# Performance work log

Hardware: AMD Instinct MI355X
Metric: run time of the kernel (lower is better)

Reference implementation:

```python
import jax, jax.numpy as jnp
import numpy as np

D_MODEL, N_HEADS, D_K = 768, 12, 64
LN_EPS = 1e-5


def setup_inputs() -> dict:
    key = jax.random.key(0)
    ks = jax.random.split(key, 8)
    b, c, n, s = 8, 32, 4, 64
    scale = 1.0 / np.sqrt(D_MODEL)
    inp = {
        "e": jax.random.normal(ks[0], (b, c, n, s, D_MODEL), dtype=jnp.float32),
        "h": jax.random.normal(ks[1], (b, c, s, D_MODEL), dtype=jnp.float32),
        # weights stored [in, out] (torch Linear transposed)
        "Wq": jax.random.normal(ks[2], (D_MODEL, N_HEADS * D_K), dtype=jnp.float32) * scale,
        "bq": jnp.zeros((N_HEADS * D_K,), dtype=jnp.float32),
        "Wk": jax.random.normal(ks[3], (D_MODEL, N_HEADS * D_K), dtype=jnp.float32) * scale,
        "bk": jnp.zeros((N_HEADS * D_K,), dtype=jnp.float32),
        "Wv": jax.random.normal(ks[4], (D_MODEL, N_HEADS * D_K), dtype=jnp.float32) * scale,
        "bv": jnp.zeros((N_HEADS * D_K,), dtype=jnp.float32),
        "Wo": jax.random.normal(ks[5], (N_HEADS * D_K, D_MODEL), dtype=jnp.float32) * scale,
        "bo": jnp.zeros((D_MODEL,), dtype=jnp.float32),
        "ln_g": jnp.ones((D_MODEL,), dtype=jnp.float32),
        "ln_b": jnp.zeros((D_MODEL,), dtype=jnp.float32),
    }
    return inp


def _layer_norm(x, g, b):
    mu = jnp.mean(x, axis=-1, keepdims=True)
    var = jnp.mean(jnp.square(x - mu), axis=-1, keepdims=True)
    return (x - mu) * jax.lax.rsqrt(var + LN_EPS) * g + b


def reference(e, h, Wq, bq, Wk, bk, Wv, bv, Wo, bo, ln_g, ln_b):
    # e: [b, c, n, i, d]  h: [b, c, j, d]
    e_res = e
    en = _layer_norm(e, ln_g, ln_b)
    b, c, n, i, _ = e.shape
    j = h.shape[2]
    q = (en @ Wq + bq).reshape(b, c, n, i, N_HEADS, D_K)
    k = (h @ Wk + bk).reshape(b, c, j, N_HEADS, D_K)
    v = (h @ Wv + bv).reshape(b, c, j, N_HEADS, D_K)
    attn = jnp.einsum('bcnihd,bcjhd->bcnhij', q, k) * (1.0 / np.sqrt(D_K))
    attn = jax.nn.softmax(attn, axis=-1)
    o = jnp.einsum('bcnhij,bcjhd->bcnihd', attn, v).reshape(b, c, n, i, N_HEADS * D_K)
    return o @ Wo + bo + e_res
```

## Files before the change

### kernel.cpp

```cpp
#include <hip/hip_runtime.h>

typedef __bf16 bf16x8 __attribute__((ext_vector_type(8)));
typedef __bf16 bf16x4 __attribute__((ext_vector_type(4)));
typedef float f32x4 __attribute__((ext_vector_type(4)));

__device__ __forceinline__ f32x4 mfma16(bf16x8 a, bf16x8 b, f32x4 c) {
  return __builtin_amdgcn_mfma_f32_16x16x32_bf16(a, b, c, 0, 0, 0);
}

__device__ __forceinline__ void load_lds16(const void* g, void* l) {
  __builtin_amdgcn_global_load_lds(
      (const __attribute__((address_space(1))) void*)g,
      (__attribute__((address_space(3))) void*)l, 16, 0, 0);
}

template <int NWG>
__device__ __forceinline__ int xcd_swz(int orig) {
  constexpr int NX = 8;
  constexpr int q = NWG / NX;
  constexpr int r = NWG % NX;
  const int xcd = orig % NX;
  const int pos = orig / NX;
  if constexpr (r == 0) {
    return xcd * q + pos;
  } else {
    return (xcd < r ? xcd * (q + 1) : r * (q + 1) + (xcd - r) * q) + pos;
  }
}

__global__ __launch_bounds__(256) void prep_w_kernel(
    const float* __restrict__ Wq, const float* __restrict__ Wk,
    const float* __restrict__ Wv, const float* __restrict__ Wo,
    __bf16* __restrict__ WqT, __bf16* __restrict__ WkvT, __bf16* __restrict__ WoT) {
  __shared__ float tile[32][33];
  const int z = blockIdx.z;
  const float* W = (z == 0) ? Wq : (z == 1) ? Wk : (z == 2) ? Wv : Wo;
  __bf16* out = (z == 0) ? WqT : (z == 3) ? WoT : WkvT;
  const int rowOff = (z == 2) ? 768 : 0;
  const int tx = threadIdx.x, ty = threadIdx.y;
  const int x = blockIdx.x * 32 + tx;
  const int y = blockIdx.y * 32 + ty;
#pragma unroll
  for (int i = 0; i < 32; i += 8) tile[ty + i][tx] = W[(size_t)(y + i) * 768 + x];
  __syncthreads();
  const int nx = blockIdx.y * 32 + tx;
  const int ny = blockIdx.x * 32 + ty;
#pragma unroll
  for (int i = 0; i < 32; i += 8)
    out[(size_t)(rowOff + ny + i) * 768 + nx] = (__bf16)tile[tx][ty + i];
}

__global__ __launch_bounds__(256) void ln_kernel(
    const float* __restrict__ e, const float* __restrict__ gam,
    const float* __restrict__ bet, __bf16* __restrict__ en) {
  const int lane = threadIdx.x & 63;
  const int wid = threadIdx.x >> 6;
  const size_t row = (size_t)blockIdx.x * 4 + wid;
  const float* p = e + row * 768;
  float x[12];
  float sum = 0.f;
#pragma unroll
  for (int s = 0; s < 3; ++s) {
    f32x4 v = *(const f32x4*)(p + (s * 64 + lane) * 4);
#pragma unroll
    for (int q = 0; q < 4; ++q) { x[s * 4 + q] = v[q]; sum += v[q]; }
  }
#pragma unroll
  for (int d = 1; d < 64; d <<= 1) sum += __shfl_xor(sum, d);
  const float m = sum * (1.f / 768.f);
  float vs = 0.f;
#pragma unroll
  for (int q = 0; q < 12; ++q) { float d = x[q] - m; vs += d * d; }
#pragma unroll
  for (int d = 1; d < 64; d <<= 1) vs += __shfl_xor(vs, d);
  const float rr = rsqrtf(vs * (1.f / 768.f) + 1e-5f);
  __bf16* o = en + row * 768;
#pragma unroll
  for (int s = 0; s < 3; ++s) {
    f32x4 g4 = *(const f32x4*)(gam + (s * 64 + lane) * 4);
    f32x4 b4 = *(const f32x4*)(bet + (s * 64 + lane) * 4);
    bf16x4 pk;
#pragma unroll
    for (int q = 0; q < 4; ++q) pk[q] = (__bf16)((x[s * 4 + q] - m) * rr * g4[q] + b4[q]);
    *(bf16x4*)(o + (s * 64 + lane) * 4) = pk;
  }
}

__global__ __launch_bounds__(256) void cast_kernel(
    const float* __restrict__ in, __bf16* __restrict__ out, int n4) {
  int i = blockIdx.x * 256 + threadIdx.x;
  const int stride = gridDim.x * 256;
  for (; i < n4; i += stride) {
    f32x4 v = ((const f32x4*)in)[i];
    bf16x4 o;
#pragma unroll
    for (int q = 0; q < 4; ++q) o[q] = (__bf16)v[q];
    ((bf16x4*)out)[i] = o;
  }
}

enum { MODE_Q = 0, MODE_KV = 1, MODE_O = 2 };

template <int MODE, int NC, int NWG>
__global__ __launch_bounds__(256) void gemm_kernel(
    const __bf16* __restrict__ A,
    const __bf16* __restrict__ WT,
    const float* __restrict__ bias0, const float* __restrict__ bias1,
    const float* __restrict__ eres,
    __bf16* __restrict__ dst0, __bf16* __restrict__ dst1,
    float* __restrict__ outp) {
  __shared__ __bf16 As[2][8192];
  __shared__ __bf16 Bs[2][8192];
  const int wgid = xcd_swz<NWG>(blockIdx.x);
  const int rowBase = (wgid / NC) * 128;
  const int colBase = (wgid % NC) * 128;
  const int t = threadIdx.x;
  const int lane = t & 63, wid = t >> 6;
  const int wm = wid >> 1, wn = wid & 1;
  const int lr = lane & 15, lg = lane >> 4;
  const int srow = lane >> 3;
  const int skcol = ((lane & 7) ^ srow) * 8;
  f32x4 acc[4][4] = {};

  auto stage = [&](int kbb, int buf) {
#pragma unroll
    for (int s = 0; s < 4; ++s) {
      const int chunk = s * 4 + wid;
      const int rowIn = chunk * 8 + srow;
      const __bf16* ga;
      if constexpr (MODE == MODE_O) {
        const int r = rowBase + rowIn;
        ga = A + ((((size_t)(r >> 6)) * 12 + kbb) << 12) + ((r & 63) << 6) + skcol;
      } else {
        ga = A + (size_t)(rowBase + rowIn) * 768 + kbb * 64 + skcol;
      }
      load_lds16(ga, &As[buf][chunk * 512]);
      const __bf16* gb = WT + (size_t)(colBase + rowIn) * 768 + kbb * 64 + skcol;
      load_lds16(gb, &Bs[buf][chunk * 512]);
    }
  };
  auto compute = [&](int buf) {
#pragma unroll
    for (int kc = 0; kc < 2; ++kc) {
      bf16x8 a[4], b[4];
      const int c8 = (kc * 4 + lg) ^ (lr & 7);
#pragma unroll
      for (int it = 0; it < 4; ++it)
        a[it] = *(const bf16x8*)&As[buf][(wm * 64 + it * 16 + lr) * 64 + c8 * 8];
#pragma unroll
      for (int jt = 0; jt < 4; ++jt)
        b[jt] = *(const bf16x8*)&Bs[buf][(wn * 64 + jt * 16 + lr) * 64 + c8 * 8];
#pragma unroll
      for (int it = 0; it < 4; ++it)
#pragma unroll
        for (int jt = 0; jt < 4; ++jt)
          acc[it][jt] = mfma16(a[it], b[jt], acc[it][jt]);
    }
  };

  stage(0, 0);
  stage(1, 1);
#pragma unroll
  for (int kb = 0; kb < 12; ++kb) {
    if (kb < 11) {
      asm volatile("s_waitcnt vmcnt(8)" ::: "memory");
    } else {
      asm volatile("s_waitcnt vmcnt(0)" ::: "memory");
    }
    __builtin_amdgcn_sched_barrier(0);
    __builtin_amdgcn_s_barrier();
    compute(kb & 1);
    __builtin_amdgcn_s_barrier();
    if (kb < 10) stage(kb + 2, kb & 1);
  }

  const int roww = rowBase + wm * 64;
  const int colw = colBase + wn * 64;
#pragma unroll
  for (int it = 0; it < 4; ++it) {
#pragma unroll
    for (int jt = 0; jt < 4; ++jt) {
      const int c = colw + jt * 16 + lr;
#pragma unroll
      for (int rg = 0; rg < 4; ++rg) {
        const int r = roww + it * 16 + lg * 4 + rg;
        const float val = acc[it][jt][rg];
        if constexpr (MODE == MODE_O) {
          outp[(size_t)r * 768 + c] = val + bias0[c] + eres[(size_t)r * 768 + c];
        } else if constexpr (MODE == MODE_Q) {
          dst0[((((size_t)(r >> 6)) * 12 + (c >> 6)) << 12) + ((r & 63) << 6) + (c & 63)] =
              (__bf16)(val + bias0[c]);
        } else {
          if (c < 768) {
            dst0[((((size_t)(r >> 6)) * 12 + (c >> 6)) << 12) + ((r & 63) << 6) + (c & 63)] =
                (__bf16)(val + bias0[c]);
          } else {
            const int c2 = c - 768;
            dst1[((((size_t)(r >> 6)) * 12 + (c2 >> 6)) << 12) + ((c2 & 63) << 6) + (r & 63)] =
                (__bf16)(val + bias1[c2]);
          }
        }
      }
    }
  }
}

__global__ __launch_bounds__(64) void attn_kernel(
    const __bf16* __restrict__ q, const __bf16* __restrict__ k,
    const __bf16* __restrict__ v, __bf16* __restrict__ o) {
  const int gid = xcd_swz<12288>(blockIdx.x);
  const int n = gid & 3;
  const int bh = gid >> 2;
  const int h = bh % 12;
  const int bc = bh / 12;
  const __bf16* qp = q + (((size_t)(bc * 4 + n) * 12 + h) << 12);
  const __bf16* kp = k + (((size_t)bc * 12 + h) << 12);
  const __bf16* vp = v + (((size_t)bc * 12 + h) << 12);
  __bf16* op = o + (((size_t)(bc * 4 + n) * 12 + h) << 12);
  const int lane = threadIdx.x;
  const int lr = lane & 15, lg = lane >> 4;
  __shared__ __bf16 P[64][72];

  bf16x8 qf[4][2], kf[4][2];
#pragma unroll
  for (int it = 0; it < 4; ++it)
#pragma unroll
    for (int kc = 0; kc < 2; ++kc)
      qf[it][kc] = *(const bf16x8*)(qp + (it * 16 + lr) * 64 + kc * 32 + lg * 8);
#pragma unroll
  for (int jt = 0; jt < 4; ++jt)
#pragma unroll
    for (int kc = 0; kc < 2; ++kc)
      kf[jt][kc] = *(const bf16x8*)(kp + (jt * 16 + lr) * 64 + kc * 32 + lg * 8);

  f32x4 s[4][4] = {};
#pragma unroll
  for (int kc = 0; kc < 2; ++kc)
#pragma unroll
    for (int jt = 0; jt < 4; ++jt)
#pragma unroll
      for (int it = 0; it < 4; ++it)
        s[jt][it] = mfma16(kf[jt][kc], qf[it][kc], s[jt][it]);

  float recip[4];
#pragma unroll
  for (int it = 0; it < 4; ++it) {
    float m = -1e30f;
#pragma unroll
    for (int jt = 0; jt < 4; ++jt)
#pragma unroll
      for (int rg = 0; rg < 4; ++rg) m = fmaxf(m, s[jt][it][rg]);
    m = fmaxf(m, __shfl_xor(m, 16));
    m = fmaxf(m, __shfl_xor(m, 32));
    float sum = 0.f;
#pragma unroll
    for (int jt = 0; jt < 4; ++jt) {
      bf16x4 pk;
#pragma unroll
      for (int rg = 0; rg < 4; ++rg) {
        float p = __expf((s[jt][it][rg] - m) * 0.125f);
        sum += p;
        pk[rg] = (__bf16)p;
      }
      *(bf16x4*)&P[it * 16 + lr][jt * 16 + lg * 4] = pk;
    }
    sum += __shfl_xor(sum, 16);
    sum += __shfl_xor(sum, 32);
    recip[it] = 1.f / sum;
  }
  __syncthreads();

  bf16x8 vf[4][2];
#pragma unroll
  for (int dt = 0; dt < 4; ++dt)
#pragma unroll
    for (int kc = 0; kc < 2; ++kc)
      vf[dt][kc] = *(const bf16x8*)(vp + (dt * 16 + lr) * 64 + kc * 32 + lg * 8);
  f32x4 oacc[4][4] = {};
#pragma unroll
  for (int kc = 0; kc < 2; ++kc) {
    bf16x8 pf[4];
#pragma unroll
    for (int it = 0; it < 4; ++it)
      pf[it] = *(const bf16x8*)&P[it * 16 + lr][kc * 32 + lg * 8];
#pragma unroll
    for (int dt = 0; dt < 4; ++dt)
#pragma unroll
      for (int it = 0; it < 4; ++it)
        oacc[dt][it] = mfma16(vf[dt][kc], pf[it], oacc[dt][it]);
  }
#pragma unroll
  for (int it = 0; it < 4; ++it) {
    const float rc = recip[it];
#pragma unroll
    for (int dt = 0; dt < 4; ++dt) {
      bf16x4 pk;
#pragma unroll
      for (int rg = 0; rg < 4; ++rg) pk[rg] = (__bf16)(oacc[dt][it][rg] * rc);
      *(bf16x4*)(op + (size_t)(it * 16 + lr) * 64 + dt * 16 + lg * 4) = pk;
    }
  }
}

extern "C" void kernel_launch(void* const* d_in, const int* in_sizes, int n_in,
                              void* d_out, int out_size, void* d_ws, size_t ws_size,
                              hipStream_t stream) {
  const float* e  = (const float*)d_in[0];
  const float* h  = (const float*)d_in[1];
  const float* Wq = (const float*)d_in[2];
  const float* bq = (const float*)d_in[3];
  const float* Wk = (const float*)d_in[4];
  const float* bk = (const float*)d_in[5];
  const float* Wv = (const float*)d_in[6];
  const float* bv = (const float*)d_in[7];
  const float* Wo = (const float*)d_in[8];
  const float* bo = (const float*)d_in[9];
  const float* g  = (const float*)d_in[10];
  const float* b  = (const float*)d_in[11];
  float* outp = (float*)d_out;
  char* ws = (char*)d_ws;

  __bf16* WqT  = (__bf16*)(ws);
  __bf16* WkvT = (__bf16*)(ws + 1179648);
  __bf16* WoT  = (__bf16*)(ws + 3538944);
  char* R1 = ws + 4718592;
  __bf16* en    = (__bf16*)(R1);
  __bf16* h_bf  = (__bf16*)(R1);
  __bf16* k_ws  = (__bf16*)(R1 + 25165824);
  __bf16* v_ws  = (__bf16*)(R1 + 50331648);
  __bf16* q_ws  = (__bf16*)(ws + 105381888);

  prep_w_kernel<<<dim3(24, 24, 4), dim3(32, 8), 0, stream>>>(Wq, Wk, Wv, Wo, WqT, WkvT, WoT);
  ln_kernel<<<16384, 256, 0, stream>>>(e, g, b, en);
  gemm_kernel<MODE_Q, 6, 3072><<<3072, 256, 0, stream>>>(
      en, WqT, bq, nullptr, nullptr, q_ws, nullptr, nullptr);
  cast_kernel<<<2048, 256, 0, stream>>>(h, h_bf, 16384 * 768 / 4);
  gemm_kernel<MODE_KV, 12, 1536><<<1536, 256, 0, stream>>>(
      h_bf, WkvT, bk, bv, nullptr, k_ws, v_ws, nullptr);
  attn_kernel<<<12288, 64, 0, stream>>>(q_ws, k_ws, v_ws, q_ws);
  gemm_kernel<MODE_O, 6, 3072><<<3072, 256, 0, stream>>>(
      q_ws, WoT, bo, nullptr, e, nullptr, nullptr, outp);
}
```

Measured before the change: 488.6 us.

## Fuse attention with output projection into one per-(b,c,n) kernel

Replaces the separate attention kernel and the output-projection GEMM with a single kernel. Each workgroup handles one (b,c,n) row block and loops over all 12 heads, keeping the concatenated attention output in LDS, then runs the Wo GEMM with bias and residual directly from LDS. This removes the bf16 round trip of the attention output through global memory and one launch. In exchange the grid drops to 1024 workgroups with a large LDS footprint and low occupancy. Each block streams the full Wo, and the GEMM phase uses small 64x128 tiles with two barriers per k-step.

Result: slower. 638.8 us (+30.7%).

```diff
diff --git a/kernel.cpp b/kernel.cpp
--- a/kernel.cpp
+++ b/kernel.cpp
@@ -99,16 +99,14 @@
   }
 }
 
-enum { MODE_Q = 0, MODE_KV = 1, MODE_O = 2 };
+enum { MODE_Q = 0, MODE_KV = 1 };
 
 template <int MODE, int NC, int NWG>
 __global__ __launch_bounds__(256) void gemm_kernel(
     const __bf16* __restrict__ A,
     const __bf16* __restrict__ WT,
     const float* __restrict__ bias0, const float* __restrict__ bias1,
-    const float* __restrict__ eres,
-    __bf16* __restrict__ dst0, __bf16* __restrict__ dst1,
-    float* __restrict__ outp) {
+    __bf16* __restrict__ dst0, __bf16* __restrict__ dst1) {
   __shared__ __bf16 As[2][8192];
   __shared__ __bf16 Bs[2][8192];
   const int wgid = xcd_swz<NWG>(blockIdx.x);
@@ -127,13 +125,7 @@
     for (int s = 0; s < 4; ++s) {
       const int chunk = s * 4 + wid;
       const int rowIn = chunk * 8 + srow;
-      const __bf16* ga;
-      if constexpr (MODE == MODE_O) {
-        const int r = rowBase + rowIn;
-        ga = A + ((((size_t)(r >> 6)) * 12 + kbb) << 12) + ((r & 63) << 6) + skcol;
-      } else {
-        ga = A + (size_t)(rowBase + rowIn) * 768 + kbb * 64 + skcol;
-      }
+      const __bf16* ga = A + (size_t)(rowBase + rowIn) * 768 + kbb * 64 + skcol;
       load_lds16(ga, &As[buf][chunk * 512]);
       const __bf16* gb = WT + (size_t)(colBase + rowIn) * 768 + kbb * 64 + skcol;
       load_lds16(gb, &Bs[buf][chunk * 512]);
@@ -185,9 +177,7 @@
       for (int rg = 0; rg < 4; ++rg) {
         const int r = roww + it * 16 + lg * 4 + rg;
         const float val = acc[it][jt][rg];
-        if constexpr (MODE == MODE_O) {
-          outp[(size_t)r * 768 + c] = val + bias0[c] + eres[(size_t)r * 768 + c];
-        } else if constexpr (MODE == MODE_Q) {
+        if constexpr (MODE == MODE_Q) {
           dst0[((((size_t)(r >> 6)) * 12 + (c >> 6)) << 12) + ((r & 63) << 6) + (c & 63)] =
               (__bf16)(val + bias0[c]);
         } else {
@@ -205,51 +195,68 @@
   }
 }
 
-__global__ __launch_bounds__(64) void attn_kernel(
+__global__ __launch_bounds__(256) void attn_o_kernel(
     const __bf16* __restrict__ q, const __bf16* __restrict__ k,
-    const __bf16* __restrict__ v, __bf16* __restrict__ o) {
-  const int gid = xcd_swz<12288>(blockIdx.x);
-  const int n = gid & 3;
-  const int bh = gid >> 2;
-  const int h = bh % 12;
-  const int bc = bh / 12;
-  const __bf16* qp = q + (((size_t)(bc * 4 + n) * 12 + h) << 12);
-  const __bf16* kp = k + (((size_t)bc * 12 + h) << 12);
-  const __bf16* vp = v + (((size_t)bc * 12 + h) << 12);
-  __bf16* op = o + (((size_t)(bc * 4 + n) * 12 + h) << 12);
-  const int lane = threadIdx.x;
+    const __bf16* __restrict__ v, const __bf16* __restrict__ WoT,
+    const float* __restrict__ bo, const float* __restrict__ e,
+    float* __restrict__ outp) {
+  __shared__ __bf16 oL[64][776];
+  __shared__ __bf16 kL[64][72];
+  __shared__ __bf16 vL[64][72];
+  __shared__ __bf16 P[4][16][72];
+  __shared__ __bf16 Bs[128][72];
+  const int bcn = xcd_swz<1024>(blockIdx.x);
+  const int bc = bcn >> 2;
+  const int t = threadIdx.x;
+  const int wid = t >> 6, lane = t & 63;
   const int lr = lane & 15, lg = lane >> 4;
-  __shared__ __bf16 P[64][72];
-
-  bf16x8 qf[4][2], kf[4][2];
-#pragma unroll
-  for (int it = 0; it < 4; ++it)
-#pragma unroll
-    for (int kc = 0; kc < 2; ++kc)
-      qf[it][kc] = *(const bf16x8*)(qp + (it * 16 + lr) * 64 + kc * 32 + lg * 8);
-#pragma unroll
-  for (int jt = 0; jt < 4; ++jt)
-#pragma unroll
-    for (int kc = 0; kc < 2; ++kc)
-      kf[jt][kc] = *(const bf16x8*)(kp + (jt * 16 + lr) * 64 + kc * 32 + lg * 8);
-
-  f32x4 s[4][4] = {};
+  const __bf16* qbase = q + (size_t)bcn * 49152;
+  const __bf16* kbase = k + (size_t)bc * 49152;
+  const __bf16* vbase = v + (size_t)bc * 49152;
+  const int srow = t >> 3, scol = (t & 7) * 8;
+
+#pragma unroll
+  for (int s = 0; s < 2; ++s) {
+    *(bf16x8*)&kL[s * 32 + srow][scol] = *(const bf16x8*)(kbase + (s * 32 + srow) * 64 + scol);
+    *(bf16x8*)&vL[s * 32 + srow][scol] = *(const bf16x8*)(vbase + (s * 32 + srow) * 64 + scol);
+  }
+  bf16x8 qf[2];
 #pragma unroll
   for (int kc = 0; kc < 2; ++kc)
+    qf[kc] = *(const bf16x8*)(qbase + (wid * 16 + lr) * 64 + kc * 32 + lg * 8);
+  __syncthreads();
+
+  for (int h = 0; h < 12; ++h) {
+    bf16x8 kn[2], vn[2], qn[2];
+    if (h < 11) {
+      const __bf16* kp = kbase + (h + 1) * 4096;
+      const __bf16* vp = vbase + (h + 1) * 4096;
+      const __bf16* qp = qbase + (h + 1) * 4096;
+#pragma unroll
+      for (int s = 0; s < 2; ++s) {
+        kn[s] = *(const bf16x8*)(kp + (s * 32 + srow) * 64 + scol);
+        vn[s] = *(const bf16x8*)(vp + (s * 32 + srow) * 64 + scol);
+      }
+#pragma unroll
+      for (int kc = 0; kc < 2; ++kc)
+        qn[kc] = *(const bf16x8*)(qp + (wid * 16 + lr) * 64 + kc * 32 + lg * 8);
+    }
+    f32x4 s4[4] = {};
+#pragma unroll
+    for (int kc = 0; kc < 2; ++kc) {
+      bf16x8 kf[4];
+#pragma unroll
+      for (int jt = 0; jt < 4; ++jt)
+        kf[jt] = *(const bf16x8*)&kL[jt * 16 + lr][kc * 32 + lg * 8];
+#pragma unroll
+      for (int jt = 0; jt < 4; ++jt)
+        s4[jt] = mfma16(kf[jt], qf[kc], s4[jt]);
+    }
+    float m = -1e30f;
 #pragma unroll
     for (int jt = 0; jt < 4; ++jt)
 #pragma unroll
-      for (int it = 0; it < 4; ++it)
-        s[jt][it] = mfma16(kf[jt][kc], qf[it][kc], s[jt][it]);
-
-  float recip[4];
-#pragma unroll
-  for (int it = 0; it < 4; ++it) {
-    float m = -1e30f;
-#pragma unroll
-    for (int jt = 0; jt < 4; ++jt)
-#pragma unroll
-      for (int rg = 0; rg < 4; ++rg) m = fmaxf(m, s[jt][it][rg]);
+      for (int rg = 0; rg < 4; ++rg) m = fmaxf(m, s4[jt][rg]);
     m = fmaxf(m, __shfl_xor(m, 16));
     m = fmaxf(m, __shfl_xor(m, 32));
     float sum = 0.f;
@@ -258,47 +265,110 @@
       bf16x4 pk;
 #pragma unroll
       for (int rg = 0; rg < 4; ++rg) {
-        float p = __expf((s[jt][it][rg] - m) * 0.125f);
+        float p = __expf((s4[jt][rg] - m) * 0.125f);
         sum += p;
         pk[rg] = (__bf16)p;
       }
-      *(bf16x4*)&P[it * 16 + lr][jt * 16 + lg * 4] = pk;
+      *(bf16x4*)&P[wid][lr][jt * 16 + lg * 4] = pk;
     }
     sum += __shfl_xor(sum, 16);
     sum += __shfl_xor(sum, 32);
-    recip[it] = 1.f / sum;
-  }
-  __syncthreads();
-
-  bf16x8 vf[4][2];
-#pragma unroll
-  for (int dt = 0; dt < 4; ++dt)
-#pragma unroll
-    for (int kc = 0; kc < 2; ++kc)
-      vf[dt][kc] = *(const bf16x8*)(vp + (dt * 16 + lr) * 64 + kc * 32 + lg * 8);
-  f32x4 oacc[4][4] = {};
-#pragma unroll
-  for (int kc = 0; kc < 2; ++kc) {
-    bf16x8 pf[4];
-#pragma unroll
-    for (int it = 0; it < 4; ++it)
-      pf[it] = *(const bf16x8*)&P[it * 16 + lr][kc * 32 + lg * 8];
-#pragma unroll
-    for (int dt = 0; dt < 4; ++dt)
-#pragma unroll
-      for (int it = 0; it < 4; ++it)
-        oacc[dt][it] = mfma16(vf[dt][kc], pf[it], oacc[dt][it]);
-  }
-#pragma unroll
-  for (int it = 0; it < 4; ++it) {
-    const float rc = recip[it];
+    const float recip = 1.f / sum;
+    f32x4 oacc[4] = {};
+#pragma unroll
+    for (int kc = 0; kc < 2; ++kc) {
+      bf16x8 pf = *(const bf16x8*)&P[wid][lr][kc * 32 + lg * 8];
+      bf16x8 vf[4];
+#pragma unroll
+      for (int dt = 0; dt < 4; ++dt)
+        vf[dt] = *(const bf16x8*)&vL[dt * 16 + lr][kc * 32 + lg * 8];
+#pragma unroll
+      for (int dt = 0; dt < 4; ++dt)
+        oacc[dt] = mfma16(vf[dt], pf, oacc[dt]);
+    }
 #pragma unroll
     for (int dt = 0; dt < 4; ++dt) {
       bf16x4 pk;
 #pragma unroll
-      for (int rg = 0; rg < 4; ++rg) pk[rg] = (__bf16)(oacc[dt][it][rg] * rc);
-      *(bf16x4*)(op + (size_t)(it * 16 + lr) * 64 + dt * 16 + lg * 4) = pk;
-    }
+      for (int rg = 0; rg < 4; ++rg) pk[rg] = (__bf16)(oacc[dt][rg] * recip);
+      *(bf16x4*)&oL[wid * 16 + lr][h * 64 + dt * 16 + lg * 4] = pk;
+    }
+    __syncthreads();
+    if (h < 11) {
+#pragma unroll
+      for (int s = 0; s < 2; ++s) {
+        *(bf16x8*)&kL[s * 32 + srow][scol] = kn[s];
+        *(bf16x8*)&vL[s * 32 + srow][scol] = vn[s];
+      }
+      qf[0] = qn[0]; qf[1] = qn[1];
+    }
+    __syncthreads();
+  }
+
+  const int wm = wid >> 1, wn = wid & 1;
+  const size_t R0 = (size_t)bcn * 64;
+  bf16x8 Bn[4];
+#pragma unroll
+  for (int s = 0; s < 4; ++s) {
+    const int gran = s * 256 + t;
+    Bn[s] = *(const bf16x8*)(WoT + (size_t)(gran >> 3) * 768 + (gran & 7) * 8);
+  }
+#pragma unroll
+  for (int s = 0; s < 4; ++s) {
+    const int gran = s * 256 + t;
+    *(bf16x8*)&Bs[gran >> 3][(gran & 7) * 8] = Bn[s];
+  }
+  __syncthreads();
+  f32x4 acc[2][4] = {};
+  for (int g = 0; g < 72; ++g) {
+    const int c = g / 12, ks = g % 12;
+    if (g < 71) {
+      const int cn = (g + 1) / 12, ksn = (g + 1) % 12;
+#pragma unroll
+      for (int s = 0; s < 4; ++s) {
+        const int gran = s * 256 + t;
+        Bn[s] = *(const bf16x8*)(WoT + (size_t)(cn * 128 + (gran >> 3)) * 768 + ksn * 64 + (gran & 7) * 8);
+      }
+    }
+#pragma unroll
+    for (int kc = 0; kc < 2; ++kc) {
+      bf16x8 a[2], b[4];
+#pragma unroll
+      for (int it = 0; it < 2; ++it)
+        a[it] = *(const bf16x8*)&oL[wm * 32 + it * 16 + lr][ks * 64 + kc * 32 + lg * 8];
+#pragma unroll
+      for (int jt = 0; jt < 4; ++jt)
+        b[jt] = *(const bf16x8*)&Bs[wn * 64 + jt * 16 + lr][kc * 32 + lg * 8];
+#pragma unroll
+      for (int it = 0; it < 2; ++it)
+#pragma unroll
+        for (int jt = 0; jt < 4; ++jt)
+          acc[it][jt] = mfma16(a[it], b[jt], acc[it][jt]);
+    }
+    if (ks == 11) {
+#pragma unroll
+      for (int it = 0; it < 2; ++it) {
+#pragma unroll
+        for (int jt = 0; jt < 4; ++jt) {
+          const int col = c * 128 + wn * 64 + jt * 16 + lr;
+#pragma unroll
+          for (int rg = 0; rg < 4; ++rg) {
+            const int r = wm * 32 + it * 16 + lg * 4 + rg;
+            outp[(R0 + r) * 768 + col] = acc[it][jt][rg] + bo[col] + e[(R0 + r) * 768 + col];
+            acc[it][jt][rg] = 0.f;
+          }
+        }
+      }
+    }
+    __syncthreads();
+    if (g < 71) {
+#pragma unroll
+      for (int s = 0; s < 4; ++s) {
+        const int gran = s * 256 + t;
+        *(bf16x8*)&Bs[gran >> 3][(gran & 7) * 8] = Bn[s];
+      }
+    }
+    __syncthreads();
   }
 }
 
@@ -333,11 +403,9 @@
   prep_w_kernel<<<dim3(24, 24, 4), dim3(32, 8), 0, stream>>>(Wq, Wk, Wv, Wo, WqT, WkvT, WoT);
   ln_kernel<<<16384, 256, 0, stream>>>(e, g, b, en);
   gemm_kernel<MODE_Q, 6, 3072><<<3072, 256, 0, stream>>>(
-      en, WqT, bq, nullptr, nullptr, q_ws, nullptr, nullptr);
+      en, WqT, bq, nullptr, q_ws, nullptr);
   cast_kernel<<<2048, 256, 0, stream>>>(h, h_bf, 16384 * 768 / 4);
   gemm_kernel<MODE_KV, 12, 1536><<<1536, 256, 0, stream>>>(
-      h_bf, WkvT, bk, bv, nullptr, k_ws, v_ws, nullptr);
-  attn_kernel<<<12288, 64, 0, stream>>>(q_ws, k_ws, v_ws, q_ws);
-  gemm_kernel<MODE_O, 6, 3072><<<3072, 256, 0, stream>>>(
-      q_ws, WoT, bo, nullptr, e, nullptr, nullptr, outp);
-}
+      h_bf, WkvT, bk, bv, k_ws, v_ws);
+  attn_o_kernel<<<1024, 256, 0, stream>>>(q_ws, k_ws, v_ws, WoT, bo, e, outp);
+}
```
